# Kernel optimization log

Hardware: AMD Instinct MI355X
Metric: run time of the kernel (lower is better)

The kernel has to match this reference:

```python
import jax, jax.numpy as jnp
import numpy as np
import math

WS = 8      # window_size
SS = 4      # stride = window_size // 2
NHEADS = 4

def _grid(size, ws, ss):
    n = (size - ws) // ss + 1
    return jnp.arange(n)[:, None] * ss + jnp.arange(ws)[None, :]  # (n, ws)

def _unfold(x, ws, ss):
    # x: (B,C,Hp,Wp) -> (B, L, C, ws*ws), matching torch F.unfold ordering
    B, C, Hp, Wp = x.shape
    ri = _grid(Hp, ws, ss)
    ci = _grid(Wp, ws, ss)
    p = x[:, :, ri][:, :, :, :, ci]  # (B,C,nH,ws,nW,ws)
    nH, nW = ri.shape[0], ci.shape[0]
    p = p.transpose(0, 2, 4, 1, 3, 5).reshape(B, nH * nW, C, ws * ws)
    return p, nH, nW

def _fold(p, Hp, Wp, nH, nW, ws, ss):
    # p: (B, L, C, ws*ws) -> overlap-add to (B,C,Hp,Wp), matching torch F.fold
    B, L, C, _ = p.shape
    p = p.reshape(B, nH, nW, C, ws, ws).transpose(0, 3, 1, 4, 2, 5)  # (B,C,nH,ws,nW,ws)
    rr = _grid(Hp, ws, ss)[:, :, None, None]   # (nH,ws,1,1)
    cc = _grid(Wp, ws, ss)[None, None, :, :]   # (1,1,nW,ws)
    return jnp.zeros((B, C, Hp, Wp), p.dtype).at[:, :, rr, cc].add(p)

def _se(h, w1, w2):
    # squeeze-excite: global avg pool -> 1x1 reduce -> relu -> 1x1 expand -> sigmoid gate
    pooled = h.mean(axis=(2, 3))                                # (B, gc)
    s = jax.nn.sigmoid(jax.nn.relu(pooled @ w1.T) @ w2.T)       # (B, gc)
    return h * s[:, :, None, None]

def _forward(low, high, w_ql, w_kh, w_vh, w_qh, w_kl, w_vl, w_proj_l, w_proj_h,
             se0_w1, se0_w2, se1_w1, se1_w2, se2_w1, se2_w2):
    B, C, H, W = low.shape
    ws, ss = WS, SS
    n_h = 0 if H <= ws else math.ceil((H - ws) / ss)
    n_w = 0 if W <= ws else math.ceil((W - ws) / ss)
    Hp, Wp = n_h * ss + ws, n_w * ss + ws
    pad = ((0, 0), (0, 0), (0, Hp - H), (0, Wp - W))
    low_p = jnp.pad(low, pad)
    high_p = jnp.pad(high, pad)
    base, rem = divmod(C, 3)
    chs = [base + (1 if i < rem else 0) for i in range(3)]
    ofs = np.cumsum([0] + chs)
    sew = [(se0_w1, se0_w2), (se1_w1, se1_w2), (se2_w1, se2_w2)]
    high_dir = jnp.concatenate(
        [_se(high_p[:, ofs[i]:ofs[i + 1]], *sew[i]) for i in range(3)], axis=1)
    lw, nH, nW = _unfold(low_p, ws, ss)    # (B,L,C,Np)
    hw, _, _ = _unfold(high_dir, ws, ss)
    L, Np, d = lw.shape[1], ws * ws, C // NHEADS
    scale = d ** -0.5
    proj = lambda x, w: jnp.einsum('oc,blcn->blon', w, x).reshape(B, L, NHEADS, d, Np)
    a_lh = jax.nn.softmax(jnp.einsum('blhdn,blhdm->blhnm', proj(lw, w_ql), proj(hw, w_kh)) * scale, axis=-1)
    a_hl = jax.nn.softmax(jnp.einsum('blhdn,blhdm->blhnm', proj(hw, w_qh), proj(lw, w_kl)) * scale, axis=-1)
    ol = jnp.einsum('blhnm,blhdm->blhdn', a_lh, proj(hw, w_vh)).reshape(B, L, C, Np)
    oh = jnp.einsum('blhnm,blhdm->blhdn', a_hl, proj(lw, w_vl)).reshape(B, L, C, Np)
    mask = _fold(jnp.ones((1, L, 1, Np), low.dtype), Hp, Wp, nH, nW, ws, ss)  # overlap counts
    out_l = (_fold(ol, Hp, Wp, nH, nW, ws, ss) / mask)[:, :, :H, :W]
    out_h = (_fold(oh, Hp, Wp, nH, nW, ws, ss) / mask)[:, :, :H, :W]
    return (low + jnp.einsum('oc,bchw->bohw', w_proj_l, out_l),
            high + jnp.einsum('oc,bchw->bohw', w_proj_h, out_h))

def setup_inputs() -> dict:
    key = jax.random.key(0)
    ks = jax.random.split(key, 20)
    B, C, H, W = 4, 64, 128, 128
    chs = [22, 21, 21]
    d = {
        'low': jax.random.normal(ks[0], (B, C, H, W), jnp.float32),
        'high': jax.random.normal(ks[1], (B, C, H, W), jnp.float32),
    }
    for i, n in enumerate(['w_ql', 'w_kh', 'w_vh', 'w_qh', 'w_kl', 'w_vl', 'w_proj_l', 'w_proj_h']):
        d[n] = jax.random.normal(ks[2 + i], (C, C), jnp.float32) * (C ** -0.5)
    for i, gc in enumerate(chs):
        d[f'se{i}_w1'] = jax.random.normal(ks[10 + 2 * i], (1, gc), jnp.float32) * 0.1
        d[f'se{i}_w2'] = jax.random.normal(ks[11 + 2 * i], (gc, 1), jnp.float32) * 0.1
    return d

def reference(low, high, w_ql, w_kh, w_vh, w_qh, w_kl, w_vl, w_proj_l, w_proj_h,
              se0_w1, se0_w2, se1_w1, se1_w2, se2_w1, se2_w2):
    return _forward(low, high, w_ql, w_kh, w_vh, w_qh, w_kl, w_vl, w_proj_l, w_proj_h,
                    se0_w1, se0_w2, se1_w1, se1_w2, se2_w1, se2_w2)
```

## Files before the change

### kernel.cpp

```cpp
#include <hip/hip_runtime.h>

typedef short short8 __attribute__((ext_vector_type(8)));
typedef short short4v __attribute__((ext_vector_type(4)));
typedef float f4 __attribute__((ext_vector_type(4)));

#define NB 4
#define NHW 128
#define NPX (NHW*NHW)
#define NWIN 31
#define NL (NWIN*NWIN)
#define SWV(r,c) (((r)<<6) + (((((c)>>3) ^ ((r)&7))<<3) | ((c)&7)))
#define MFMA(a,b,c) __builtin_amdgcn_mfma_f32_16x16x32_bf16(a,b,c,0,0,0)

__device__ __forceinline__ short f2bf(float f) {
    unsigned u = __float_as_uint(f);
    u += 0x7fffu + ((u >> 16) & 1u);
    return (short)(u >> 16);
}
__device__ __forceinline__ short f2bft(float f) {
    return (short)(__float_as_uint(f) >> 16);
}
__device__ __forceinline__ float bf2f(short v) {
    return __uint_as_float(((unsigned)(unsigned short)v) << 16);
}

__global__ void k_pool(const float* __restrict__ high, float* __restrict__ pooled) {
    int bc = blockIdx.x;
    const float* src = high + (size_t)bc * NPX;
    float s = 0.f;
    for (int i = threadIdx.x; i < NPX; i += 256) s += src[i];
    for (int off = 32; off > 0; off >>= 1) s += __shfl_down(s, off);
    __shared__ float red[4];
    int lane = threadIdx.x & 63, wv = threadIdx.x >> 6;
    if (lane == 0) red[wv] = s;
    __syncthreads();
    if (threadIdx.x == 0)
        pooled[bc] = (red[0] + red[1] + red[2] + red[3]) * (1.f / NPX);
}

__global__ void k_gate(const float* __restrict__ pooled,
                       const float* __restrict__ w10, const float* __restrict__ w20,
                       const float* __restrict__ w11, const float* __restrict__ w21,
                       const float* __restrict__ w12, const float* __restrict__ w22,
                       const float* __restrict__ wpl, const float* __restrict__ wph,
                       float* __restrict__ sgate, short* __restrict__ wbf) {
    __shared__ float pl[256];
    int t = threadIdx.x;
    pl[t] = pooled[t];
    #pragma unroll
    for (int i = 0; i < 32; ++i) {
        int idx = t + i*256;
        const float* src = (idx < 4096) ? wpl : wph;
        wbf[idx] = f2bf(src[idx & 4095]);
    }
    __syncthreads();
    int b = t >> 6, c = t & 63;
    const float* w1; const float* w2; int o0, gc;
    if (c < 22)      { w1 = w10; w2 = w20; o0 = 0;  gc = 22; }
    else if (c < 43) { w1 = w11; w2 = w21; o0 = 22; gc = 21; }
    else             { w1 = w12; w2 = w22; o0 = 43; gc = 21; }
    float a = 0.f;
    for (int k = 0; k < gc; ++k) a += pl[b*64 + o0 + k] * w1[k];
    a = fmaxf(a, 0.f);
    float z = a * w2[c - o0];
    sgate[t] = 1.f / (1.f + __expf(-z));
}

__device__ __forceinline__ void wrange(int x, int& lo, int& hi) {
    lo = (x >= 7) ? ((x - 4) >> 2) : 0;
    hi = x >> 2; if (hi > 30) hi = 30;
}

template<int EMIT>
__device__ __forceinline__ void proj_body(
    const float* __restrict__ src, const float* __restrict__ gate,
    const float* __restrict__ Wq, const float* __restrict__ Wk, const float* __restrict__ Wv,
    short* __restrict__ Qp, short* __restrict__ Kp, short* __restrict__ Vp,
    short* T, int b, int row, int t) {
    const float* sp = src + (size_t)b*64*NPX + row*NHW;
    #pragma unroll
    for (int i = 0; i < 8; ++i) {
        int f = t + i*256;
        int c = f & 63, px = (f >> 6) << 2;
        float4 v = *(const float4*)(sp + (size_t)c*NPX + px);
        float g = gate ? gate[b*64 + c] : 1.f;
        T[SWV(px + 0, c)] = f2bf(v.x * g);
        T[SWV(px + 1, c)] = f2bf(v.y * g);
        T[SWV(px + 2, c)] = f2bf(v.z * g);
        T[SWV(px + 3, c)] = f2bf(v.w * g);
    }
    __syncthreads();
    int w = t >> 6, ln = t & 63, l16 = ln & 15, quad = ln >> 4;
    int orow = 16*w + l16;
    short8 wq[2], wk[2], wv[2];
    #pragma unroll
    for (int kf = 0; kf < 2; ++kf) {
        if (EMIT & 1) {
            const float* p = Wq + orow*64 + kf*32 + quad*8;
            #pragma unroll
            for (int j = 0; j < 8; ++j) wq[kf][j] = f2bf(p[j]);
        }
        if (EMIT & 2) {
            const float* p = Wk + orow*64 + kf*32 + quad*8;
            #pragma unroll
            for (int j = 0; j < 8; ++j) wk[kf][j] = f2bf(p[j]);
        }
        if (EMIT & 4) {
            const float* p = Wv + orow*64 + kf*32 + quad*8;
            #pragma unroll
            for (int j = 0; j < 8; ++j) wv[kf][j] = f2bf(p[j]);
        }
    }
    #pragma unroll
    for (int nt = 0; nt < 8; ++nt) {
        int px = nt*16 + l16;
        short8 xb0 = *(const short8*)(T + SWV(px, quad*8));
        short8 xb1 = *(const short8*)(T + SWV(px, 32 + quad*8));
        size_t clbase = ((size_t)b*NPX + row*NHW + px)*64 + 16*w + quad*4;
        if (EMIT & 1) {
            f4 acc = {0.f,0.f,0.f,0.f};
            acc = MFMA(wq[0], xb0, acc); acc = MFMA(wq[1], xb1, acc);
            short4v sv;
            #pragma unroll
            for (int r = 0; r < 4; ++r) sv[r] = f2bf(acc[r] * 0.25f);
            *(short4v*)(Qp + clbase) = sv;
        }
        if (EMIT & 2) {
            f4 acc = {0.f,0.f,0.f,0.f};
            acc = MFMA(wk[0], xb0, acc); acc = MFMA(wk[1], xb1, acc);
            short4v sv;
            #pragma unroll
            for (int r = 0; r < 4; ++r) sv[r] = f2bf(acc[r]);
            *(short4v*)(Kp + clbase) = sv;
        }
        if (EMIT & 4) {
            f4 acc = {0.f,0.f,0.f,0.f};
            acc = MFMA(wv[0], xb0, acc); acc = MFMA(wv[1], xb1, acc);
            #pragma unroll
            for (int r = 0; r < 4; ++r)
                Vp[((size_t)(b*64 + 16*w + quad*4 + r))*NPX + row*NHW + px] = f2bf(acc[r]);
        }
    }
}

template<int EMIT>
__global__ __launch_bounds__(256, 6) void k_proj(
    const float* __restrict__ src, const float* __restrict__ gate,
    const float* __restrict__ Wq, const float* __restrict__ Wk, const float* __restrict__ Wv,
    short* __restrict__ Qp, short* __restrict__ Kp, short* __restrict__ Vp) {
    __shared__ __align__(16) short T[8192];
    proj_body<EMIT>(src, gate, Wq, Wk, Wv, Qp, Kp, Vp, T,
                    blockIdx.x >> 7, blockIdx.x & 127, threadIdx.x);
}

__global__ __launch_bounds__(256, 6) void k_proj2(
    const float* __restrict__ s0, const float* __restrict__ s1, const float* __restrict__ gate,
    const float* __restrict__ Wq0, const float* __restrict__ Wk0, const float* __restrict__ Wv0,
    const float* __restrict__ Wq1, const float* __restrict__ Wk1, const float* __restrict__ Wv1,
    short* __restrict__ Q0, short* __restrict__ K0, short* __restrict__ V0,
    short* __restrict__ Q1, short* __restrict__ K1, short* __restrict__ V1) {
    __shared__ __align__(16) short T[8192];
    int region = blockIdx.x & 7;
    int ss = region >> 2, b = region & 3, row = blockIdx.x >> 3;
    if (ss == 0)
        proj_body<7>(s0, nullptr, Wq0, Wk0, Wv0, Q0, K0, V0, T, b, row, threadIdx.x);
    else
        proj_body<7>(s1, gate, Wq1, Wk1, Wv1, Q1, K1, V1, T, b, row, threadIdx.x);
}

template<int SWZ>
__global__ __launch_bounds__(256, 6) void k_attn(
    const short* __restrict__ Q0, const short* __restrict__ K0, const short* __restrict__ V0,
    const short* __restrict__ Q1, const short* __restrict__ K1, const short* __restrict__ V1,
    short* __restrict__ scr, size_t scr_stride, int nb) {
    __shared__ __align__(16) short Pb[4][1024];
    int bidx = blockIdx.x;
    int pass, b, l;
    if (SWZ) {
        int region = bidx & 7;
        pass = region >> 2; b = region & 3; l = bidx >> 3;
    } else {
        int per = nb * NL;
        pass = bidx / per; int rem2 = bidx - pass*per;
        b = rem2 / NL; l = rem2 - b*NL;
    }
    const short* Qp = pass ? Q1 : Q0;
    const short* Kp = pass ? K1 : K0;
    const short* Vp = pass ? V1 : V0;
    short* scrp = scr + (size_t)pass * scr_stride;
    int wr = l / NWIN, wc = l - (l/NWIN)*NWIN;
    int row0 = wr*4, col0 = wc*4;
    int parity = (wr & 1)*2 + (wc & 1);
    int t = threadIdx.x, w = t >> 6, ln = t & 63, l16 = ln & 15, quad = ln >> 4;
    int h = w;
    short* PT = Pb[w];
    short8 z = {0,0,0,0,0,0,0,0};
    const short one = (short)0x3F80;
    short8 ones = {one,one,one,one,one,one,one,one};

    short8 kb[4];
    #pragma unroll
    for (int mt = 0; mt < 4; ++mt) {
        int m = mt*16 + l16;
        int px = (row0 + (m >> 3))*NHW + col0 + (m & 7);
        kb[mt] = (quad < 2) ? *(const short8*)(Kp + ((size_t)b*NPX + px)*64 + h*16 + quad*8) : z;
    }
    short8 va0, va1;
    {
        const short* vb = Vp + ((size_t)(b*64 + h*16 + l16))*NPX;
        const short* p0 = vb + (row0 + quad)*NHW + col0;
        const short* p1 = vb + (row0 + 4 + quad)*NHW + col0;
        short4v a = *(const short4v*)p0, bq = *(const short4v*)(p0 + 4);
        short4v c = *(const short4v*)p1, d = *(const short4v*)(p1 + 4);
        #pragma unroll
        for (int j = 0; j < 4; ++j) { va0[j] = a[j]; va0[4+j] = bq[j]; va1[j] = c[j]; va1[4+j] = d[j]; }
    }

    #pragma unroll
    for (int ntl = 0; ntl < 4; ++ntl) {
        int n = ntl*16 + l16;
        int px = (row0 + (n >> 3))*NHW + col0 + (n & 7);
        short8 qa = (quad < 2) ? *(const short8*)(Qp + ((size_t)b*NPX + px)*64 + h*16 + quad*8) : z;
        f4 s[4];
        #pragma unroll
        for (int mt = 0; mt < 4; ++mt) {
            f4 acc = {0.f,0.f,0.f,0.f};
            s[mt] = MFMA(qa, kb[mt], acc);
        }
        #pragma unroll
        for (int mt = 0; mt < 4; ++mt)
            #pragma unroll
            for (int r = 0; r < 4; ++r)
                PT[SWV(quad*4 + r, mt*16 + l16)] = f2bft(__expf(fminf(s[mt][r], 30.f)));
        short8 pb0 = *(const short8*)(PT + SWV(l16, quad*8));
        short8 pb1 = *(const short8*)(PT + SWV(l16, 32 + quad*8));
        f4 o = {0.f,0.f,0.f,0.f};
        o = MFMA(va0, pb0, o);
        o = MFMA(va1, pb1, o);
        f4 dn = {0.f,0.f,0.f,0.f};
        dn = MFMA(ones, pb0, dn);
        dn = MFMA(ones, pb1, dn);
        float inv = __builtin_amdgcn_rcpf(dn[0]);
        short4v sv;
        #pragma unroll
        for (int r = 0; r < 4; ++r) sv[r] = f2bf(o[r] * inv);
        *(short4v*)(scrp + (((size_t)(parity*nb + b))*NPX + px)*64 + h*16 + quad*4) = sv;
    }
}

template<int SWZ>
__global__ __launch_bounds__(256, 4) void k_gather(
    const short* __restrict__ scr, size_t scr_stride,
    const float* __restrict__ r0, const float* __restrict__ r1,
    const short* __restrict__ wpb,
    float* __restrict__ o0, float* __restrict__ o1, int nb) {
    int bidx = blockIdx.x;
    int pass, b, hh, half;
    if (SWZ) {
        int region = bidx & 7;
        pass = region >> 2; b = region & 3;
        int rem2 = bidx >> 3; hh = rem2 >> 1; half = rem2 & 1;
    } else {
        pass = 0;
        b = bidx / (NHW*2); int rem2 = bidx - b*(NHW*2);
        hh = rem2 >> 1; half = rem2 & 1;
    }
    const short* scrp = scr + (size_t)pass * scr_stride;
    const float* resid = pass ? r1 : r0;
    const short* wproj = wpb + (SWZ ? pass*4096 : 0);
    float* outp = pass ? o1 : o0;
    int t = threadIdx.x, w = t >> 6, ln = t & 63, l16 = ln & 15, quad = ln >> 4;
    int px = half*64 + w*16 + l16;
    int rlo, rhi, clo, chi;
    wrange(hh, rlo, rhi); wrange(px, clo, chi);
    bool okr0 = (rhi > rlo) || ((rlo & 1) == 0);
    bool okr1 = (rhi > rlo) || ((rlo & 1) == 1);
    bool okc0 = (chi > clo) || ((clo & 1) == 0);
    bool okc1 = (chi > clo) || ((clo & 1) == 1);
    short8 wa[4][2];
    #pragma unroll
    for (int ct = 0; ct < 4; ++ct)
        #pragma unroll
        for (int kf = 0; kf < 2; ++kf)
            wa[ct][kf] = *(const short8*)(wproj + (ct*16 + l16)*64 + kf*32 + quad*8);
    f4 acc[4];
    #pragma unroll
    for (int ct = 0; ct < 4; ++ct) acc[ct] = (f4){0.f,0.f,0.f,0.f};
    short8 z = {0,0,0,0,0,0,0,0};
    #pragma unroll
    for (int par = 0; par < 4; ++par) {
        bool valid = ((par >> 1) ? okr1 : okr0) && ((par & 1) ? okc1 : okc0);
        const short* sp2 = scrp + (((size_t)(par*nb + b))*NPX + hh*NHW + px)*64;
        short8 b0 = *(const short8*)(sp2 + quad*8);
        short8 b1 = *(const short8*)(sp2 + 32 + quad*8);
        if (!valid) { b0 = z; b1 = z; }
        #pragma unroll
        for (int ct = 0; ct < 4; ++ct) {
            acc[ct] = MFMA(wa[ct][0], b0, acc[ct]);
            acc[ct] = MFMA(wa[ct][1], b1, acc[ct]);
        }
    }
    float inv = 1.f / ((float)(rhi - rlo + 1) * (float)(chi - clo + 1));
    #pragma unroll
    for (int ct = 0; ct < 4; ++ct)
        #pragma unroll
        for (int r = 0; r < 4; ++r) {
            size_t gi = (((size_t)(b*64 + ct*16 + quad*4 + r))*NHW + hh)*NHW + px;
            outp[gi] = resid[gi] + acc[ct][r] * inv;
        }
}

extern "C" void kernel_launch(void* const* d_in, const int* in_sizes, int n_in,
                              void* d_out, int out_size, void* d_ws, size_t ws_size,
                              hipStream_t stream) {
    const float* low  = (const float*)d_in[0];
    const float* high = (const float*)d_in[1];
    const float* w_ql = (const float*)d_in[2];
    const float* w_kh = (const float*)d_in[3];
    const float* w_vh = (const float*)d_in[4];
    const float* w_qh = (const float*)d_in[5];
    const float* w_kl = (const float*)d_in[6];
    const float* w_vl = (const float*)d_in[7];
    const float* w_pl = (const float*)d_in[8];
    const float* w_ph = (const float*)d_in[9];
    float* out = (float*)d_out;
    float* pooled = (float*)d_ws;
    float* sgate  = pooled + 256;
    short* wbf = (short*)((char*)d_ws + 2048);
    short* base = wbf + 8192;
    const size_t PL = (size_t)NB * NPX * 64;
    const size_t plane_f = (size_t)NB * 64 * NPX;
    const size_t SCR = 4 * PL;
    const size_t HDR = 2048 + 8192*sizeof(short);
    size_t need_fused  = HDR + (6*PL + 2*SCR) * sizeof(short);
    size_t need_serial = HDR + (6*PL + SCR) * sizeof(short);
    size_t scr_elems_per_b = 4 * (size_t)NPX * 64;

    k_pool<<<dim3(NB*64), dim3(256), 0, stream>>>(high, pooled);
    k_gate<<<dim3(1), dim3(256), 0, stream>>>(pooled,
        (const float*)d_in[10], (const float*)d_in[11],
        (const float*)d_in[12], (const float*)d_in[13],
        (const float*)d_in[14], (const float*)d_in[15],
        w_pl, w_ph, sgate, wbf);

    if (ws_size >= need_serial) {
        short* QL = base;        short* KL = base + PL;   short* VL = base + 2*PL;
        short* QH = base + 3*PL; short* KH = base + 4*PL; short* VH = base + 5*PL;
        short* scr = base + 6*PL;
        k_proj2<<<dim3(8*NHW), dim3(256), 0, stream>>>(low, high, sgate,
            w_ql, w_kl, w_vl, w_qh, w_kh, w_vh,
            QL, KL, VL, QH, KH, VH);
        if (ws_size >= need_fused) {
            k_attn<1><<<dim3(8*NL), dim3(256), 0, stream>>>(QL, KH, VH, QH, KL, VL, scr, SCR, NB);
            k_gather<1><<<dim3(8*NHW*2), dim3(256), 0, stream>>>(scr, SCR, low, high,
                wbf, out, out + plane_f, NB);
        } else {
            k_attn<0><<<dim3(NB*NL), dim3(256), 0, stream>>>(QL, KH, VH, nullptr, nullptr, nullptr, scr, 0, NB);
            k_gather<0><<<dim3(NB*NHW*2), dim3(256), 0, stream>>>(scr, 0, low, nullptr,
                wbf, out, nullptr, NB);
            k_attn<0><<<dim3(NB*NL), dim3(256), 0, stream>>>(QH, KL, VL, nullptr, nullptr, nullptr, scr, 0, NB);
            k_gather<0><<<dim3(NB*NHW*2), dim3(256), 0, stream>>>(scr, 0, high, nullptr,
                wbf + 4096, out + plane_f, nullptr, NB);
        }
    } else {
        short* P0 = base; short* P1 = base + PL; short* P2 = base + 2*PL;
        short* scr = base + 3*PL;
        int nbc = 0;
        for (int n = NB; n >= 1; n >>= 1)
            if (ws_size >= HDR + (3*PL + n*scr_elems_per_b)*sizeof(short)) { nbc = n; break; }
        if (nbc == 0) nbc = 1;
        for (int pass = 0; pass < 2; ++pass) {
            const float* qsrc = pass ? high : low;
            const float* ksrc = pass ? low  : high;
            const float* qg   = pass ? sgate : nullptr;
            const float* kg   = pass ? nullptr : sgate;
            const float* Wq   = pass ? w_qh : w_ql;
            const float* Wk   = pass ? w_kl : w_kh;
            const float* Wv   = pass ? w_vl : w_vh;
            const short* Wpb  = wbf + pass*4096;
            const float* resid = pass ? high : low;
            float* op = out + (size_t)pass * plane_f;
            k_proj<1><<<dim3(NB*NHW), dim3(256), 0, stream>>>(qsrc, qg, Wq, nullptr, nullptr, P0, nullptr, nullptr);
            k_proj<6><<<dim3(NB*NHW), dim3(256), 0, stream>>>(ksrc, kg, nullptr, Wk, Wv, nullptr, P1, P2);
            for (int b0 = 0; b0 < NB; b0 += nbc) {
                int nb = (NB - b0) < nbc ? (NB - b0) : nbc;
                size_t boff = (size_t)b0 * NPX * 64;
                k_attn<0><<<dim3(nb*NL), dim3(256), 0, stream>>>(P0 + boff, P1 + boff, P2 + boff,
                    nullptr, nullptr, nullptr, scr, 0, nb);
                k_gather<0><<<dim3(nb*NHW*2), dim3(256), 0, stream>>>(scr, 0, resid + boff, nullptr,
                    Wpb, op + boff, nullptr, nb);
            }
        }
    }
}
```

Measured before the change: 224.0 us.

## Vectorize pooling loads, LDS transpose stores, and raise gather occupancy

The pooling kernel now reads float4 vectors instead of scalars. The projection staging now reads four channels per pixel and writes them to shared memory as one packed 4-short store instead of four scalar stores. The attention score MFMA swaps its operands so each lane's exp results land contiguously and can be written as one short4 store to the probability tile. The gather kernel's launch bounds ask for 6 waves per SIMD instead of 4, which caps registers and risks spills.

```diff
diff --git a/kernel.cpp b/kernel.cpp
--- a/kernel.cpp
+++ b/kernel.cpp
@@ -26,9 +26,12 @@
 
 __global__ void k_pool(const float* __restrict__ high, float* __restrict__ pooled) {
     int bc = blockIdx.x;
-    const float* src = high + (size_t)bc * NPX;
+    const float4* src = (const float4*)(high + (size_t)bc * NPX);
     float s = 0.f;
-    for (int i = threadIdx.x; i < NPX; i += 256) s += src[i];
+    for (int i = threadIdx.x; i < NPX/4; i += 256) {
+        float4 v = src[i];
+        s += (v.x + v.y) + (v.z + v.w);
+    }
     for (int off = 32; off > 0; off >>= 1) s += __shfl_down(s, off);
     __shared__ float red[4];
     int lane = threadIdx.x & 63, wv = threadIdx.x >> 6;
@@ -81,13 +84,15 @@
     #pragma unroll
     for (int i = 0; i < 8; ++i) {
         int f = t + i*256;
-        int c = f & 63, px = (f >> 6) << 2;
-        float4 v = *(const float4*)(sp + (size_t)c*NPX + px);
-        float g = gate ? gate[b*64 + c] : 1.f;
-        T[SWV(px + 0, c)] = f2bf(v.x * g);
-        T[SWV(px + 1, c)] = f2bf(v.y * g);
-        T[SWV(px + 2, c)] = f2bf(v.z * g);
-        T[SWV(px + 3, c)] = f2bf(v.w * g);
+        int px = f & 127, c4 = (f >> 7) << 2;
+        short4v sv;
+        #pragma unroll
+        for (int j = 0; j < 4; ++j) {
+            float v = sp[(size_t)(c4 + j)*NPX + px];
+            if (gate) v *= gate[b*64 + c4 + j];
+            sv[j] = f2bf(v);
+        }
+        *(short4v*)(T + SWV(px, c4)) = sv;
     }
     __syncthreads();
     int w = t >> 6, ln = t & 63, l16 = ln & 15, quad = ln >> 4;
@@ -221,17 +226,16 @@
         int n = ntl*16 + l16;
         int px = (row0 + (n >> 3))*NHW + col0 + (n & 7);
         short8 qa = (quad < 2) ? *(const short8*)(Qp + ((size_t)b*NPX + px)*64 + h*16 + quad*8) : z;
-        f4 s[4];
         #pragma unroll
         for (int mt = 0; mt < 4; ++mt) {
-            f4 acc = {0.f,0.f,0.f,0.f};
-            s[mt] = MFMA(qa, kb[mt], acc);
-        }
-        #pragma unroll
-        for (int mt = 0; mt < 4; ++mt)
+            f4 zz = {0.f,0.f,0.f,0.f};
+            f4 s = MFMA(kb[mt], qa, zz);
+            short4v pv;
             #pragma unroll
             for (int r = 0; r < 4; ++r)
-                PT[SWV(quad*4 + r, mt*16 + l16)] = f2bft(__expf(fminf(s[mt][r], 30.f)));
+                pv[r] = f2bft(__expf(fminf(s[r], 30.f)));
+            *(short4v*)(PT + SWV(l16, mt*16 + quad*4)) = pv;
+        }
         short8 pb0 = *(const short8*)(PT + SWV(l16, quad*8));
         short8 pb1 = *(const short8*)(PT + SWV(l16, 32 + quad*8));
         f4 o = {0.f,0.f,0.f,0.f};
@@ -249,7 +253,7 @@
 }
 
 template<int SWZ>
-__global__ __launch_bounds__(256, 4) void k_gather(
+__global__ __launch_bounds__(256, 6) void k_gather(
     const short* __restrict__ scr, size_t scr_stride,
     const float* __restrict__ r0, const float* __restrict__ r1,
     const short* __restrict__ wpb,
```

After: 208.2 us. 7.1% less time.
